# Performance work log

Hardware: AMD Instinct MI355X
Metric: run time of the kernel (lower is better)

## Reference

```python
import jax, jax.numpy as jnp
import numpy as np

# conv_ada hyperparameters from init_kwargs: ka=1, alpha=0.25, kw=0.2
KA1 = 1.0          # activation scale for conv1 (ka)
KA2 = 1.25         # activation scale for conv2 (ka + alpha)
KW = 0.2           # weight clipping threshold used by the binary weight STE


def ste_sign(x, clip=1.0):
    """Binary sign with straight-through estimator (hardtanh-style clip).
    Forward value is sign(x); gradient is that of clip(x, -clip, clip)."""
    xc = jnp.clip(x, -clip, clip)
    return xc + jax.lax.stop_gradient(jnp.sign(x) - xc)


def conv_bin(x, w, ka, kw):
    """1-bit activation / 1-bit weight 3x3 conv (conv_ada).
    Activations -> ka * sign(x); weights -> per-out-channel mean(|w|) * sign(w)."""
    xq = ka * ste_sign(x)
    alpha_w = jnp.mean(jnp.abs(w), axis=(1, 2, 3), keepdims=True)  # [O,1,1,1]
    wq = alpha_w * ste_sign(w, kw)
    return jax.lax.conv_general_dilated(
        xq, wq, window_strides=(1, 1), padding='SAME',
        dimension_numbers=('NCHW', 'OIHW', 'NCHW'))


def prelu(x, slope):
    # per-channel PReLU, slope shape [C]
    return jnp.where(x >= 0, x, slope[None, :, None, None] * x)


def pixel_shuffle(x, r=2):
    b, c, h, w = x.shape
    co = c // (r * r)
    x = x.reshape(b, co, r, r, h, w)
    x = x.transpose(0, 1, 4, 2, 5, 3)  # b, co, h, r, w, r
    return x.reshape(b, co, h * r, w * r)


def setup_inputs() -> dict:
    key = jax.random.key(0)
    ks = jax.random.split(key, 11)
    B, C, H, W = 8, 64, 256, 256
    return {
        'x': jax.random.normal(ks[0], (B, C, H, W), jnp.float32),
        'w1': jax.random.normal(ks[1], (C, C, 3, 3), jnp.float32) * 0.1,
        'w2': jax.random.normal(ks[2], (2 * C, C, 3, 3), jnp.float32) * 0.1,
        'b_in': jax.random.normal(ks[3], (1, C, 1, 1), jnp.float32) * 0.01,
        'b1': jax.random.normal(ks[4], (1, C, 1, 1), jnp.float32) * 0.01,
        's1': jax.random.uniform(ks[5], (C,), jnp.float32) * 0.25,
        'b2': jax.random.normal(ks[6], (1, C, 1, 1), jnp.float32) * 0.01,
        'b2_': jax.random.normal(ks[7], (1, C, 1, 1), jnp.float32) * 0.01,
        'b3': jax.random.normal(ks[8], (1, 2 * C, 1, 1), jnp.float32) * 0.01,
        's2': jax.random.uniform(ks[9], (2 * C,), jnp.float32) * 0.25,
        'b4': jax.random.normal(ks[10], (1, 2 * C, 1, 1), jnp.float32) * 0.01,
    }


def reference(x, w1, w2, b_in, b1, s1, b2, b2_, b3, s2, b4):
    out = conv_bin(x + b_in, w1, KA1, KW)       # move1_ -> conv1
    xres = out + x                              # residual x = out + x
    # NOTE: in the original forward, move1 -> prelu1 -> move2 are computed on
    # `out` and then immediately overwritten by out = move2_(x); that branch
    # is dead code and does not affect the output (b1, s1, b2 get zero grads).
    out = conv_bin(xres + b2_, w2, KA2, KW)     # move2_ -> conv2
    out = out + jnp.concatenate([xres, xres], axis=1)  # shortcut = cat(x, x)
    out = prelu(out + b3, s2) + b4              # move3 -> prelu2 -> move4
    return pixel_shuffle(out, 2)                # [B, C/2, 2H, 2W]
```

## Files before the change

### kernel.cpp

```cpp
#include <hip/hip_runtime.h>
#include <hip/hip_bf16.h>

typedef unsigned long long u64;
typedef unsigned int u32;
typedef unsigned short ushort8 __attribute__((ext_vector_type(8)));
typedef u64 u64x2 __attribute__((ext_vector_type(2)));
typedef u64 u64x4 __attribute__((ext_vector_type(4)));
typedef float fx2 __attribute__((ext_vector_type(2)));
typedef float fx4 __attribute__((ext_vector_type(4)));

#define IMG_H 256
#define IMG_W 256
#define CIN   64
#define HW    (IMG_H * IMG_W)
#define NPIX  (8 * HW)

static __device__ __forceinline__ float bf16bits_to_f32(unsigned short h) {
    union { u32 u; float f; } c;
    c.u = ((u32)h) << 16;
    return c.f;
}
static __device__ __forceinline__ unsigned short f32_to_bf16bits(float f) {
    __hip_bfloat16 hb = __float2bfloat16(f);
    return *(unsigned short*)&hb;
}

__global__ void prep_kernel(const float* __restrict__ w1,
                            const float* __restrict__ w2,
                            u64* __restrict__ w1b, float* __restrict__ a1,
                            u64* __restrict__ w2b, float* __restrict__ a2) {
    int blk = blockIdx.x;
    int lane = threadIdx.x;
    const float* w;
    u64* wb;
    float* al;
    if (blk < 64) { w = w1 + (size_t)blk * 576;        wb = w1b + blk * 9;        al = a1 + blk; }
    else          { w = w2 + (size_t)(blk - 64) * 576; wb = w2b + (blk - 64) * 9; al = a2 + (blk - 64); }

    const float* wi = w + lane * 9;
    float s = 0.f;
    u64 bits[9];
#pragma unroll
    for (int t = 0; t < 9; ++t) {
        float v = wi[t];
        s += fabsf(v);
        bits[t] = __ballot(v > 0.f);
    }
#pragma unroll
    for (int m = 32; m >= 1; m >>= 1) s += __shfl_xor(s, m);
    if (lane == 0) {
        *al = s * (1.f / 576.f);
#pragma unroll
        for (int t = 0; t < 9; ++t) wb[t] = bits[t];
    }
}

__global__ __launch_bounds__(256)
void pack_kernel(const float* __restrict__ x,
                 const float* __restrict__ b_in,
                 u64* __restrict__ bits1) {
    int tid = blockIdx.x * 256 + threadIdx.x;
    int n = tid >> 14;
    int p = (tid & 16383) * 4;
    const float* xp = x + (size_t)n * CIN * HW + p;
    u32 lo[4] = {0, 0, 0, 0}, hi[4] = {0, 0, 0, 0};
#pragma unroll
    for (int c = 0; c < 32; ++c) {
        fx4 v = *(const fx4*)(xp + (size_t)c * HW);
        float b = b_in[c];
#pragma unroll
        for (int q = 0; q < 4; ++q) lo[q] |= (u32)((v[q] + b) > 0.f) << c;
    }
#pragma unroll
    for (int c = 0; c < 32; ++c) {
        fx4 v = *(const fx4*)(xp + (size_t)(c + 32) * HW);
        float b = b_in[c + 32];
#pragma unroll
        for (int q = 0; q < 4; ++q) hi[q] |= (u32)((v[q] + b) > 0.f) << c;
    }
    u64x4 pk;
#pragma unroll
    for (int q = 0; q < 4; ++q) pk[q] = ((u64)hi[q] << 32) | lo[q];
    *(u64x4*)(bits1 + (size_t)n * HW + p) = pk;
}

__global__ __launch_bounds__(256)
void conv1_kernel(const float* __restrict__ x,
                  const float* __restrict__ b2_,
                  const u64* __restrict__ bits1,
                  const u64* __restrict__ wbits,
                  const float* __restrict__ alpha1,
                  ushort8* __restrict__ xres,
                  u64* __restrict__ bits2) {
    int i = blockIdx.x * 256 + threadIdx.x;
    int n = i >> 16, p = i & 65535;
    int y = p >> 8, xc = p & 255;

    u64 xb[9];
    int invmask = 0, nv = 0;
#pragma unroll
    for (int t = 0; t < 9; ++t) {
        int dy = t / 3 - 1, dx = t % 3 - 1;
        bool v = ((unsigned)(y + dy) < (unsigned)IMG_H) &
                 ((unsigned)(xc + dx) < (unsigned)IMG_W);
        xb[t] = v ? bits1[i + dy * IMG_W + dx] : 0ull;
        invmask |= (v ? 0 : 1) << t;
        nv += v ? 1 : 0;
    }

    const float* xp = x + (size_t)n * CIN * HW + p;
    u64 w2 = 0;

    float rvA[8], rvB[8];

    auto load_rv = [&](float* buf, int g) {
#pragma unroll
        for (int j = 0; j < 8; ++j)
            buf[j] = xp[(size_t)(g * 8 + j) * HW];
    };
    auto comp = [&](const float* buf, int g) {
        ushort8 pk;
        u32 gm = 0;
#pragma unroll
        for (int j = 0; j < 8; ++j) {
            int o = g * 8 + j;
            const u64* wo = wbits + o * 9;
            int D = 0;
#pragma unroll
            for (int t = 0; t < 9; ++t) D += __popcll(xb[t] ^ wo[t]);
            int S = 64 * nv - 2 * D;
            if (invmask) {
#pragma unroll
                for (int t = 0; t < 9; ++t)
                    if ((invmask >> t) & 1) S += 2 * __popcll(wo[t]);
            }
            float r = alpha1[o] * (float)S + buf[j];
            pk[j] = f32_to_bf16bits(r);
            gm |= (u32)((r + b2_[o]) > 0.f) << j;
        }
        xres[(size_t)(n * 8 + g) * HW + p] = pk;
        w2 |= (u64)gm << (8 * g);
    };

    load_rv(rvA, 0);
#pragma unroll 1
    for (int gg = 0; gg < 4; ++gg) {
        load_rv(rvB, 2 * gg + 1);
        comp(rvA, 2 * gg);
        if (gg < 3) load_rv(rvA, 2 * gg + 2);
        comp(rvB, 2 * gg + 1);
    }
    bits2[i] = w2;
}

__global__ __launch_bounds__(256)
void conv2_kernel(const ushort8* __restrict__ xres,
                  const u64* __restrict__ bits2,
                  const u64* __restrict__ wbits,
                  const float* __restrict__ alpha2,
                  const float* __restrict__ b3,
                  const float* __restrict__ s2,
                  const float* __restrict__ b4,
                  float* __restrict__ out) {
    int i = blockIdx.x * 256 + threadIdx.x;
    int n = i >> 16, p = i & 65535;
    int y = p >> 8, xc = p & 255;

    u64 xb[9];
    int invmask = 0, nv = 0;
#pragma unroll
    for (int t = 0; t < 9; ++t) {
        int dy = t / 3 - 1, dx = t % 3 - 1;
        bool v = ((unsigned)(y + dy) < (unsigned)IMG_H) &
                 ((unsigned)(xc + dx) < (unsigned)IMG_W);
        xb[t] = v ? bits2[i + dy * IMG_W + dx] : 0ull;
        invmask |= (v ? 0 : 1) << t;
        nv += v ? 1 : 0;
    }

    float* ob = out + (size_t)n * 32 * 512 * 512;
    const int Y = 2 * y, X = 2 * xc;
    const ushort8* xrp = xres + (size_t)n * 8 * HW + p;

    ushort8 xrA, xrB;

    auto comp = [&](ushort8 xr, int g) {
        float vlo[8], vhi[8];
#pragma unroll
        for (int j = 0; j < 8; ++j) {
            int o = g * 8 + j;
            float xrv = bf16bits_to_f32(xr[j]);
            {
                const u64* wo = wbits + o * 9;
                int D = 0;
#pragma unroll
                for (int t = 0; t < 9; ++t) D += __popcll(xb[t] ^ wo[t]);
                int S = 64 * nv - 2 * D;
                if (invmask) {
#pragma unroll
                    for (int t = 0; t < 9; ++t)
                        if ((invmask >> t) & 1) S += 2 * __popcll(wo[t]);
                }
                float u = 1.25f * alpha2[o] * (float)S + xrv + b3[o];
                u = (u >= 0.f) ? u : s2[o] * u;
                vlo[j] = u + b4[o];
            }
            {
                int o2 = o + 64;
                const u64* wo = wbits + o2 * 9;
                int D = 0;
#pragma unroll
                for (int t = 0; t < 9; ++t) D += __popcll(xb[t] ^ wo[t]);
                int S = 64 * nv - 2 * D;
                if (invmask) {
#pragma unroll
                    for (int t = 0; t < 9; ++t)
                        if ((invmask >> t) & 1) S += 2 * __popcll(wo[t]);
                }
                float u = 1.25f * alpha2[o2] * (float)S + xrv + b3[o2];
                u = (u >= 0.f) ? u : s2[o2] * u;
                vhi[j] = u + b4[o2];
            }
        }
#pragma unroll
        for (int jj = 0; jj < 8; jj += 2) {
            int o = g * 8 + jj;
            int co = o >> 2;
            int r1 = (o >> 1) & 1;
            fx2 vl; vl.x = vlo[jj]; vl.y = vlo[jj + 1];
            fx2 vh; vh.x = vhi[jj]; vh.y = vhi[jj + 1];
            __builtin_nontemporal_store(
                vl, (fx2*)(ob + ((size_t)co * 512 + Y + r1) * 512 + X));
            __builtin_nontemporal_store(
                vh, (fx2*)(ob + ((size_t)(co + 16) * 512 + Y + r1) * 512 + X));
        }
    };

    xrA = xrp[0];
#pragma unroll 1
    for (int gg = 0; gg < 4; ++gg) {
        xrB = xrp[(size_t)(2 * gg + 1) * HW];
        comp(xrA, 2 * gg);
        if (gg < 3) xrA = xrp[(size_t)(2 * gg + 2) * HW];
        comp(xrB, 2 * gg + 1);
    }
}

extern "C" void kernel_launch(void* const* d_in, const int* in_sizes, int n_in,
                              void* d_out, int out_size, void* d_ws, size_t ws_size,
                              hipStream_t stream) {
    const float* x    = (const float*)d_in[0];
    const float* w1   = (const float*)d_in[1];
    const float* w2   = (const float*)d_in[2];
    const float* b_in = (const float*)d_in[3];
    const float* b2_  = (const float*)d_in[7];
    const float* b3   = (const float*)d_in[8];
    const float* s2   = (const float*)d_in[9];
    const float* b4   = (const float*)d_in[10];
    float* out = (float*)d_out;

    char* ws = (char*)d_ws;
    u64*   w1b   = (u64*)(ws + 0);
    u64*   w2b   = (u64*)(ws + 4608);
    float* a1    = (float*)(ws + 13824);
    float* a2    = (float*)(ws + 14080);
    u64*   bits1 = (u64*)(ws + 16384);
    u64*   bits2 = (u64*)(ws + 16384 + 4194304);
    ushort8* xres = (ushort8*)(ws + 16384 + 2 * 4194304);

    prep_kernel<<<192, 64, 0, stream>>>(w1, w2, w1b, a1, w2b, a2);

    pack_kernel <<<NPIX / 1024, 256, 0, stream>>>(x, b_in, bits1);
    conv1_kernel<<<NPIX / 256, 256, 0, stream>>>(x, b2_, bits1, w1b, a1, xres, bits2);
    conv2_kernel<<<NPIX / 256, 256, 0, stream>>>(xres, bits2, w2b, a2, b3, s2, b4, out);
}
```

Before: 216.0 us.

## Process two adjacent pixels per thread in conv2 with shared bit window

conv2 now gives each thread two horizontally adjacent pixels. It loads a 3x4 window of packed activation bits once and reuses each weight word for both pixels. The output stores widen from float2 to float4, and the xres loads read 16 bf16 values at once. This cuts redundant neighbour and weight loads and widens the store transactions, at the cost of more registers and half as many threads.

```diff
diff --git a/kernel.cpp b/kernel.cpp
--- a/kernel.cpp
+++ b/kernel.cpp
@@ -4,6 +4,7 @@
 typedef unsigned long long u64;
 typedef unsigned int u32;
 typedef unsigned short ushort8 __attribute__((ext_vector_type(8)));
+typedef unsigned short ushortx16 __attribute__((ext_vector_type(16)));
 typedef u64 u64x2 __attribute__((ext_vector_type(2)));
 typedef u64 u64x4 __attribute__((ext_vector_type(4)));
 typedef float fx2 __attribute__((ext_vector_type(2)));
@@ -162,86 +163,126 @@
                   const float* __restrict__ s2,
                   const float* __restrict__ b4,
                   float* __restrict__ out) {
-    int i = blockIdx.x * 256 + threadIdx.x;
-    int n = i >> 16, p = i & 65535;
+    int tid = blockIdx.x * 256 + threadIdx.x;
+    int n = tid >> 15;
+    int p = (tid & 32767) * 2;
     int y = p >> 8, xc = p & 255;
 
-    u64 xb[9];
-    int invmask = 0, nv = 0;
+    u64 W[3][4];
+    const u64* bp = bits2 + (size_t)n * HW;
+#pragma unroll
+    for (int r = 0; r < 3; ++r) {
+        int yy = y - 1 + r;
+        bool rv = (unsigned)yy < (unsigned)IMG_H;
+        const u64* row = bp + yy * IMG_W + xc;
+        W[r][0] = (rv && xc > 0)   ? row[-1] : 0ull;
+        W[r][1] = rv ? row[0] : 0ull;
+        W[r][2] = rv ? row[1] : 0ull;
+        W[r][3] = (rv && xc < 254) ? row[2]  : 0ull;
+    }
+    int inv0 = 0, inv1 = 0, nv0 = 0, nv1 = 0;
 #pragma unroll
     for (int t = 0; t < 9; ++t) {
-        int dy = t / 3 - 1, dx = t % 3 - 1;
-        bool v = ((unsigned)(y + dy) < (unsigned)IMG_H) &
-                 ((unsigned)(xc + dx) < (unsigned)IMG_W);
-        xb[t] = v ? bits2[i + dy * IMG_W + dx] : 0ull;
-        invmask |= (v ? 0 : 1) << t;
-        nv += v ? 1 : 0;
-    }
-
+        const int r = t / 3, c = t % 3;
+        bool rv = (unsigned)(y - 1 + r) < (unsigned)IMG_H;
+        bool v0 = rv && !(c == 0 && xc == 0);
+        bool v1 = rv && !(c == 2 && xc == 254);
+        inv0 |= (v0 ? 0 : 1) << t; nv0 += v0 ? 1 : 0;
+        inv1 |= (v1 ? 0 : 1) << t; nv1 += v1 ? 1 : 0;
+    }
+    const int edge = inv0 | inv1;
+
+    const ushortx16* xrp = (const ushortx16*)(xres + (size_t)n * 8 * HW + p);
     float* ob = out + (size_t)n * 32 * 512 * 512;
     const int Y = 2 * y, X = 2 * xc;
-    const ushort8* xrp = xres + (size_t)n * 8 * HW + p;
-
-    ushort8 xrA, xrB;
-
-    auto comp = [&](ushort8 xr, int g) {
-        float vlo[8], vhi[8];
-#pragma unroll
-        for (int j = 0; j < 8; ++j) {
-            int o = g * 8 + j;
-            float xrv = bf16bits_to_f32(xr[j]);
-            {
-                const u64* wo = wbits + o * 9;
-                int D = 0;
-#pragma unroll
-                for (int t = 0; t < 9; ++t) D += __popcll(xb[t] ^ wo[t]);
-                int S = 64 * nv - 2 * D;
-                if (invmask) {
-#pragma unroll
-                    for (int t = 0; t < 9; ++t)
-                        if ((invmask >> t) & 1) S += 2 * __popcll(wo[t]);
+
+    ushortx16 xrA, xrB;
+
+    auto comp = [&](const ushortx16& xr, int g) {
+#pragma unroll
+        for (int jj = 0; jj < 8; jj += 2) {
+            float lo4[4], hi4[4];
+#pragma unroll
+            for (int q = 0; q < 2; ++q) {
+                int o = g * 8 + jj + q;
+                float xrv0 = bf16bits_to_f32(xr[jj + q]);
+                float xrv1 = bf16bits_to_f32(xr[8 + jj + q]);
+                {
+                    const u64* wo = wbits + o * 9;
+                    int D0 = 0, D1 = 0;
+#pragma unroll
+                    for (int t = 0; t < 9; ++t) {
+                        const int r = t / 3, c = t % 3;
+                        u64 w = wo[t];
+                        D0 += __popcll(W[r][c] ^ w);
+                        D1 += __popcll(W[r][c + 1] ^ w);
+                    }
+                    int S0 = 64 * nv0 - 2 * D0;
+                    int S1 = 64 * nv1 - 2 * D1;
+                    if (edge) {
+#pragma unroll
+                        for (int t = 0; t < 9; ++t) {
+                            int pw = __popcll(wo[t]);
+                            if ((inv0 >> t) & 1) S0 += 2 * pw;
+                            if ((inv1 >> t) & 1) S1 += 2 * pw;
+                        }
+                    }
+                    float ka = 1.25f * alpha2[o], bb = b3[o], ss = s2[o], b4v = b4[o];
+                    float u0 = ka * (float)S0 + xrv0 + bb;
+                    float u1 = ka * (float)S1 + xrv1 + bb;
+                    u0 = (u0 >= 0.f) ? u0 : ss * u0;
+                    u1 = (u1 >= 0.f) ? u1 : ss * u1;
+                    lo4[q] = u0 + b4v;
+                    lo4[2 + q] = u1 + b4v;
                 }
-                float u = 1.25f * alpha2[o] * (float)S + xrv + b3[o];
-                u = (u >= 0.f) ? u : s2[o] * u;
-                vlo[j] = u + b4[o];
+                {
+                    int o2 = o + 64;
+                    const u64* wo = wbits + o2 * 9;
+                    int D0 = 0, D1 = 0;
+#pragma unroll
+                    for (int t = 0; t < 9; ++t) {
+                        const int r = t / 3, c = t % 3;
+                        u64 w = wo[t];
+                        D0 += __popcll(W[r][c] ^ w);
+                        D1 += __popcll(W[r][c + 1] ^ w);
+                    }
+                    int S0 = 64 * nv0 - 2 * D0;
+                    int S1 = 64 * nv1 - 2 * D1;
+                    if (edge) {
+#pragma unroll
+                        for (int t = 0; t < 9; ++t) {
+                            int pw = __popcll(wo[t]);
+                            if ((inv0 >> t) & 1) S0 += 2 * pw;
+                            if ((inv1 >> t) & 1) S1 += 2 * pw;
+                        }
+                    }
+                    float ka = 1.25f * alpha2[o2], bb = b3[o2], ss = s2[o2], b4v = b4[o2];
+                    float u0 = ka * (float)S0 + xrv0 + bb;
+                    float u1 = ka * (float)S1 + xrv1 + bb;
+                    u0 = (u0 >= 0.f) ? u0 : ss * u0;
+                    u1 = (u1 >= 0.f) ? u1 : ss * u1;
+                    hi4[q] = u0 + b4v;
+                    hi4[2 + q] = u1 + b4v;
+                }
             }
-            {
-                int o2 = o + 64;
-                const u64* wo = wbits + o2 * 9;
-                int D = 0;
-#pragma unroll
-                for (int t = 0; t < 9; ++t) D += __popcll(xb[t] ^ wo[t]);
-                int S = 64 * nv - 2 * D;
-                if (invmask) {
-#pragma unroll
-                    for (int t = 0; t < 9; ++t)
-                        if ((invmask >> t) & 1) S += 2 * __popcll(wo[t]);
-                }
-                float u = 1.25f * alpha2[o2] * (float)S + xrv + b3[o2];
-                u = (u >= 0.f) ? u : s2[o2] * u;
-                vhi[j] = u + b4[o2];
-            }
-        }
-#pragma unroll
-        for (int jj = 0; jj < 8; jj += 2) {
             int o = g * 8 + jj;
             int co = o >> 2;
             int r1 = (o >> 1) & 1;
-            fx2 vl; vl.x = vlo[jj]; vl.y = vlo[jj + 1];
-            fx2 vh; vh.x = vhi[jj]; vh.y = vhi[jj + 1];
+            fx4 vl; vl.x = lo4[0]; vl.y = lo4[1]; vl.z = lo4[2]; vl.w = lo4[3];
+            fx4 vh; vh.x = hi4[0]; vh.y = hi4[1]; vh.z = hi4[2]; vh.w = hi4[3];
             __builtin_nontemporal_store(
-                vl, (fx2*)(ob + ((size_t)co * 512 + Y + r1) * 512 + X));
+                vl, (fx4*)(ob + ((size_t)co * 512 + Y + r1) * 512 + X));
             __builtin_nontemporal_store(
-                vh, (fx2*)(ob + ((size_t)(co + 16) * 512 + Y + r1) * 512 + X));
+                vh, (fx4*)(ob + ((size_t)(co + 16) * 512 + Y + r1) * 512 + X));
         }
     };
 
     xrA = xrp[0];
 #pragma unroll 1
     for (int gg = 0; gg < 4; ++gg) {
-        xrB = xrp[(size_t)(2 * gg + 1) * HW];
+        xrB = xrp[(size_t)(2 * gg + 1) * (HW / 2)];
         comp(xrA, 2 * gg);
-        if (gg < 3) xrA = xrp[(size_t)(2 * gg + 2) * HW];
+        if (gg < 3) xrA = xrp[(size_t)(2 * gg + 2) * (HW / 2)];
         comp(xrB, 2 * gg + 1);
     }
 }
@@ -272,5 +313,5 @@
 
     pack_kernel <<<NPIX / 1024, 256, 0, stream>>>(x, b_in, bits1);
     conv1_kernel<<<NPIX / 256, 256, 0, stream>>>(x, b2_, bits1, w1b, a1, xres, bits2);
-    conv2_kernel<<<NPIX / 256, 256, 0, stream>>>(xres, bits2, w2b, a2, b3, s2, b4, out);
-}
+    conv2_kernel<<<NPIX / 512, 256, 0, stream>>>(xres, bits2, w2b, a2, b3, s2, b4, out);
+}
```

Result: faster. 204.6 us (-5.3%).
